# Kernel optimization log

Measured on AMD Instinct MI355X. Metric: run time of the kernel, lower is better.

Reference implementation:

```python
import jax, jax.numpy as jnp
import numpy as np

EMB = 300      # LEN_EMB_VECTOR
FH, FO = 200, 200
GH, GO = 200, 200
HH, HO = 200, 3

def _mlp2(x, w1, b1, w2, b2):
    # relu(Linear) -> relu(Linear), torch Linear: y = x @ W.T + b
    h = jax.nn.relu(x @ w1.T + b1)
    return jax.nn.relu(h @ w2.T + b2)

def setup_inputs() -> dict:
    key = jax.random.key(0)
    ks = jax.random.split(key, 16)
    L1, L2 = 8192, 8192
    def lin(k, out_d, in_d):
        kw, kb = jax.random.split(k)
        s = 1.0 / np.sqrt(in_d)
        w = jax.random.uniform(kw, (out_d, in_d), jnp.float32, -s, s)
        b = jax.random.uniform(kb, (out_d,), jnp.float32, -s, s)
        return w, b
    F_w1, F_b1 = lin(ks[0], FH, EMB)
    F_w2, F_b2 = lin(ks[1], FO, FH)
    G_w1, G_b1 = lin(ks[2], GH, 2 * EMB)
    G_w2, G_b2 = lin(ks[3], GO, GH)
    H_w1, H_b1 = lin(ks[4], HH, 2 * GO)
    H_w2, H_b2 = lin(ks[5], HO, HH)
    sen1 = jax.random.normal(ks[6], (L1, EMB), jnp.float32)
    sen2 = jax.random.normal(ks[7], (L2, EMB), jnp.float32)
    return {"sen1": sen1, "sen2": sen2,
            "F_w1": F_w1, "F_b1": F_b1, "F_w2": F_w2, "F_b2": F_b2,
            "G_w1": G_w1, "G_b1": G_b1, "G_w2": G_w2, "G_b2": G_b2,
            "H_w1": H_w1, "H_b1": H_b1, "H_w2": H_w2, "H_b2": H_b2}

def reference(sen1, sen2, F_w1, F_b1, F_w2, F_b2,
              G_w1, G_b1, G_w2, G_b2, H_w1, H_b1, H_w2, H_b2):
    # F projection of every token in both sentences
    Fa = _mlp2(sen1, F_w1, F_b1, F_w2, F_b2)   # [L1, 200]
    Fb = _mlp2(sen2, F_w1, F_b1, F_w2, F_b2)   # [L2, 200]
    # E matrix of dot products: e_ij = Fa_i . Fb_j
    E = jnp.einsum('id,jd->ij', Fa, Fb)        # [L1, L2]
    # beta_i = softmax over j of E[i, :] applied to sen2
    beta = jax.nn.softmax(E, axis=1) @ sen2    # [L1, EMB]
    # alpha_j = softmax over i of E[:, j] applied to sen1
    alpha = jax.nn.softmax(E, axis=0).T @ sen1 # [L2, EMB]
    # G comparison
    v1 = _mlp2(jnp.concatenate([sen1, beta], axis=-1), G_w1, G_b1, G_w2, G_b2)   # [L1, 200]
    v2 = _mlp2(jnp.concatenate([sen2, alpha], axis=-1), G_w1, G_b1, G_w2, G_b2)  # [L2, 200]
    # aggregate: elementwise sums over tokens, then H classifier with softmax
    hx = jnp.concatenate([v1.sum(axis=0), v2.sum(axis=0)])  # [400]
    logits = jax.nn.relu(hx @ H_w1.T + H_b1) @ H_w2.T + H_b2  # [3]
    return jax.nn.softmax(logits)
```

## Files before the change

kernel.cpp:

```cpp
#include <hip/hip_runtime.h>

typedef __attribute__((ext_vector_type(8))) short short8;
typedef __attribute__((ext_vector_type(4))) float f32x4;

__device__ inline ushort f2bf(float f) {
    union { float f; unsigned u; } v{f};
    unsigned r = v.u + 0x7FFF + ((v.u >> 16) & 1);
    return (ushort)(r >> 16);
}
__device__ inline float bf2f(ushort u) {
    union { unsigned u; float f; } v;
    v.u = ((unsigned)u) << 16;
    return v.f;
}

__device__ inline void gload_lds16(const void* g, void* l) {
    __builtin_amdgcn_global_load_lds(
        (const __attribute__((address_space(1))) unsigned int*)(uintptr_t)g,
        (__attribute__((address_space(3))) unsigned int*)(uintptr_t)l,
        16, 0, 0);
}

__global__ __launch_bounds__(256) void prep_kernel(
    const float* __restrict__ s1, const float* __restrict__ s2,
    const float* __restrict__ W0, const float* __restrict__ b0,
    const float* __restrict__ W1, const float* __restrict__ b1,
    const float* __restrict__ W2, const float* __restrict__ b2,
    const float* __restrict__ W3, const float* __restrict__ b3,
    ushort* __restrict__ Senb, ushort* __restrict__ St1, ushort* __restrict__ St2,
    ushort* __restrict__ Wb0, float* __restrict__ bp0,
    ushort* __restrict__ Wb1, float* __restrict__ bp1,
    ushort* __restrict__ Wb2, float* __restrict__ bp2,
    ushort* __restrict__ Wb3, float* __restrict__ bp3)
{
    const int bid = blockIdx.x;
    if (bid < 896) {
        const int mat = bid / 224, n = bid % 224;
        if (mat == 2) {
            for (int k = threadIdx.x; k < 640; k += 256) {
                float v = 0.f;
                if (n < 200) {
                    if (k < 320) { if (k < 300) v = W2[(size_t)n * 600 + k]; }
                    else { int cc = k - 320; if (cc < 300) v = W2[(size_t)n * 600 + 300 + cc]; }
                }
                Wb2[(size_t)n * 640 + k] = f2bf(v);
            }
            if (threadIdx.x == 0) bp2[n] = (n < 200) ? b2[n] : 0.f;
            return;
        }
        const float* W; const float* b; ushort* Wb; float* bp; int N, K, KP;
        if (mat == 0)      { W = W0; b = b0; Wb = Wb0; bp = bp0; N = 200; K = 300; KP = 320; }
        else if (mat == 1) { W = W1; b = b1; Wb = Wb1; bp = bp1; N = 200; K = 200; KP = 224; }
        else               { W = W3; b = b3; Wb = Wb3; bp = bp3; N = 200; K = 200; KP = 224; }
        for (int k = threadIdx.x; k < KP; k += 256)
            Wb[(size_t)n * KP + k] = (n < N && k < K) ? f2bf(W[(size_t)n * K + k]) : (ushort)0;
        if (threadIdx.x == 0) bp[n] = (n < N) ? b[n] : 0.f;
        return;
    }
    const int sb = bid - 896;
    const int gx = sb & 127;
    const int rest = sb >> 7;
    const int gy = rest % 5, gz = rest / 5;
    const float* X = gz ? s2 : s1;
    ushort* Xt = gz ? St2 : St1;
    ushort* Sb = Senb + (size_t)gz * 8192 * 320;
    __shared__ float t[64][65];
    const int r0 = gx * 64, c0 = gy * 64;
    const int tc = threadIdx.x & 63, tr = threadIdx.x >> 6;
    for (int rr = tr; rr < 64; rr += 4) {
        int c = c0 + tc;
        float v = (c < 300) ? X[(size_t)(r0 + rr) * 300 + c] : 0.f;
        t[rr][tc] = v;
        if (c < 320) Sb[(size_t)(r0 + rr) * 320 + c] = f2bf(v);
    }
    __syncthreads();
    for (int rr = tr; rr < 64; rr += 4) {
        int oc = c0 + rr;
        if (oc < 320)
            Xt[(size_t)oc * 8192 + r0 + tc] = f2bf(t[tc][rr]);
    }
}

__global__ __launch_bounds__(128) void mlp2_kernel(
    const ushort* __restrict__ X,
    const ushort* __restrict__ W1, const float* __restrict__ b1,
    const ushort* __restrict__ W2, const float* __restrict__ b2,
    ushort* __restrict__ Ybf)
{
    const int r0 = blockIdx.x * 16;
    const int tid = threadIdx.x;
    const int wv = tid >> 6;
    const int lane = tid & 63;
    const int lr = lane & 15, lg = lane >> 4;

    __shared__ __align__(16) ushort Y1[16][232];
    __shared__ __align__(16) ushort Pp[16][224];

    f32x4 a1[14];
#pragma unroll
    for (int t = 0; t < 14; ++t) a1[t] = f32x4{0.f, 0.f, 0.f, 0.f};

    const ushort* Xrow = X + (size_t)(r0 + lr) * 320 + lg * 8;
    const ushort* W1r  = W1 + (size_t)lr * 320 + lg * 8;
    const int kb1 = wv * 160;
    for (int k0 = kb1; k0 < kb1 + 160; k0 += 32) {
        short8 a = *(const short8*)(Xrow + k0);
#pragma unroll
        for (int t = 0; t < 14; ++t) {
            short8 bfr = *(const short8*)(W1r + (size_t)t * 16 * 320 + k0);
            a1[t] = __builtin_amdgcn_mfma_f32_16x16x32_bf16(a, bfr, a1[t], 0, 0, 0);
        }
    }
    if (wv == 1) {
#pragma unroll
        for (int t = 0; t < 14; ++t)
#pragma unroll
            for (int rr = 0; rr < 4; ++rr)
                Pp[lg * 4 + rr][t * 16 + lr] = f2bf(a1[t][rr]);
    }
    __syncthreads();
    if (wv == 0) {
#pragma unroll
        for (int t = 0; t < 14; ++t) {
            int col = t * 16 + lr;
            float bv = b1[col];
#pragma unroll
            for (int rr = 0; rr < 4; ++rr) {
                float v = a1[t][rr] + bf2f(Pp[lg * 4 + rr][col]) + bv;
                Y1[lg * 4 + rr][col] = f2bf(fmaxf(v, 0.f));
            }
        }
    }
    __syncthreads();

    f32x4 a2[14];
#pragma unroll
    for (int t = 0; t < 14; ++t) a2[t] = f32x4{0.f, 0.f, 0.f, 0.f};
    const ushort* W2r = W2 + (size_t)lr * 224 + lg * 8;
    const int kb2 = wv * 128, ke2 = wv ? 224 : 128;
    for (int k0 = kb2; k0 < ke2; k0 += 32) {
        short8 a = *(const short8*)&Y1[lr][lg * 8 + k0];
#pragma unroll
        for (int t = 0; t < 14; ++t) {
            short8 bfr = *(const short8*)(W2r + (size_t)t * 16 * 224 + k0);
            a2[t] = __builtin_amdgcn_mfma_f32_16x16x32_bf16(a, bfr, a2[t], 0, 0, 0);
        }
    }
    if (wv == 1) {
#pragma unroll
        for (int t = 0; t < 14; ++t)
#pragma unroll
            for (int rr = 0; rr < 4; ++rr)
                Pp[lg * 4 + rr][t * 16 + lr] = f2bf(a2[t][rr]);
    }
    __syncthreads();
    if (wv == 0) {
#pragma unroll
        for (int t = 0; t < 14; ++t) {
            int col = t * 16 + lr;
            float bv = b2[col];
#pragma unroll
            for (int rr = 0; rr < 4; ++rr) {
                int row = r0 + lg * 4 + rr;
                float v = a2[t][rr] + bf2f(Pp[lg * 4 + rr][col]) + bv;
                Ybf[(size_t)row * 224 + col] = f2bf(fmaxf(v, 0.f));
            }
        }
    }
}

__global__ __launch_bounds__(128) void gmlp2_kernel(
    const ushort* __restrict__ Senb,
    const ushort* __restrict__ Pacc, const float* __restrict__ Dpart,
    const ushort* __restrict__ W1, const float* __restrict__ b1,
    const ushort* __restrict__ W2, const float* __restrict__ b2,
    float* __restrict__ Part)
{
    const int r0 = blockIdx.x * 16;
    const int tid = threadIdx.x;
    const int wv = tid >> 6;
    const int lane = tid & 63;
    const int lr = lane & 15, lg = lane >> 4;
    const int row = r0 + lr;

    __shared__ __align__(16) ushort Y1[16][232];
    __shared__ __align__(16) ushort Pp[16][224];

    f32x4 a1[14];
#pragma unroll
    for (int t = 0; t < 14; ++t) a1[t] = f32x4{0.f, 0.f, 0.f, 0.f};

    const ushort* W1r = W1 + (size_t)lr * 640 + lg * 8;
    if (wv == 0) {
        const ushort* Xrow = Senb + (size_t)row * 320 + lg * 8;
        for (int k0 = 0; k0 < 320; k0 += 32) {
            short8 a = *(const short8*)(Xrow + k0);
#pragma unroll
            for (int t = 0; t < 14; ++t) {
                short8 bfr = *(const short8*)(W1r + (size_t)t * 16 * 640 + k0);
                a1[t] = __builtin_amdgcn_mfma_f32_16x16x32_bf16(a, bfr, a1[t], 0, 0, 0);
            }
        }
    } else {
        const float inv = 1.f / (Dpart[row] + Dpart[16384 + row]);
        const ushort* pa = Pacc + (size_t)row * 320;
        const ushort* pb = pa + (size_t)16384 * 320;
        for (int k0 = 320; k0 < 640; k0 += 32) {
            int kk = k0 - 320 + lg * 8;
            short8 x = *(const short8*)(pa + kk);
            short8 y = *(const short8*)(pb + kk);
            short8 a;
#pragma unroll
            for (int m = 0; m < 8; ++m)
                a[m] = (short)f2bf((bf2f((ushort)x[m]) + bf2f((ushort)y[m])) * inv);
#pragma unroll
            for (int t = 0; t < 14; ++t) {
                short8 bfr = *(const short8*)(W1r + (size_t)t * 16 * 640 + k0);
                a1[t] = __builtin_amdgcn_mfma_f32_16x16x32_bf16(a, bfr, a1[t], 0, 0, 0);
            }
        }
    }
    if (wv == 1) {
#pragma unroll
        for (int t = 0; t < 14; ++t)
#pragma unroll
            for (int rr = 0; rr < 4; ++rr)
                Pp[lg * 4 + rr][t * 16 + lr] = f2bf(a1[t][rr]);
    }
    __syncthreads();
    if (wv == 0) {
#pragma unroll
        for (int t = 0; t < 14; ++t) {
            int col = t * 16 + lr;
            float bv = b1[col];
#pragma unroll
            for (int rr = 0; rr < 4; ++rr) {
                float v = a1[t][rr] + bf2f(Pp[lg * 4 + rr][col]) + bv;
                Y1[lg * 4 + rr][col] = f2bf(fmaxf(v, 0.f));
            }
        }
    }
    __syncthreads();

    f32x4 a2[14];
#pragma unroll
    for (int t = 0; t < 14; ++t) a2[t] = f32x4{0.f, 0.f, 0.f, 0.f};
    const ushort* W2r = W2 + (size_t)lr * 224 + lg * 8;
    const int kb2 = wv * 128, ke2 = wv ? 224 : 128;
    for (int k0 = kb2; k0 < ke2; k0 += 32) {
        short8 a = *(const short8*)&Y1[lr][lg * 8 + k0];
#pragma unroll
        for (int t = 0; t < 14; ++t) {
            short8 bfr = *(const short8*)(W2r + (size_t)t * 16 * 224 + k0);
            a2[t] = __builtin_amdgcn_mfma_f32_16x16x32_bf16(a, bfr, a2[t], 0, 0, 0);
        }
    }
    if (wv == 1) {
#pragma unroll
        for (int t = 0; t < 14; ++t)
#pragma unroll
            for (int rr = 0; rr < 4; ++rr)
                Pp[lg * 4 + rr][t * 16 + lr] = f2bf(a2[t][rr]);
    }
    __syncthreads();
    if (wv == 0) {
#pragma unroll
        for (int t = 0; t < 14; ++t) {
            int col = t * 16 + lr;
            if (col < 200) {
                float bv = b2[col];
                float s = 0.f;
#pragma unroll
                for (int rr = 0; rr < 4; ++rr) {
                    float v = a2[t][rr] + bf2f(Pp[lg * 4 + rr][col]) + bv;
                    s += fmaxf(v, 0.f);
                }
                s += __shfl_xor(s, 16);
                s += __shfl_xor(s, 32);
                if (lg == 0)
                    Part[(size_t)blockIdx.x * 200 + col] = s;
            }
        }
    }
}

__global__ __launch_bounds__(512, 2) void attend_mfma_kernel(
    const ushort* __restrict__ FaFb, const ushort* __restrict__ St1,
    const ushort* __restrict__ St2, ushort* __restrict__ Pacc,
    float* __restrict__ Dpart)
{
    const int b = blockIdx.x;
    const int it  = b & 63;
    const int jh  = (b >> 6) & 1;
    const int dir = b >> 7;
    const ushort* A  = FaFb + (dir ? (size_t)8192 * 224 : 0);
    const ushort* B  = FaFb + (dir ? 0 : (size_t)8192 * 224);
    const ushort* St = dir ? St1 : St2;
    const int ib = it * 128;
    const int jo = jh * 4096;

    const int tid = threadIdx.x;
    const int w = tid >> 6;
    const int wi = w >> 1, wj = w & 1;
    const int dq = w & 3,  ih = w >> 2;
    const int lane = tid & 63;
    const int lr = lane & 15, lg = lane >> 4;

    __shared__ __align__(16) ushort Bl[2][28 * 512];
    __shared__ __align__(16) ushort Sl[2][40 * 512];
    __shared__ __align__(16) ushort Pl[128][76];
    __shared__ float dled[8][32];

    f32x4 acc[4][5];
#pragma unroll
    for (int s = 0; s < 4; ++s)
#pragma unroll
        for (int t = 0; t < 5; ++t) acc[s][t] = f32x4{0.f, 0.f, 0.f, 0.f};
    float dsum[2] = {0.f, 0.f};

    short8 afr[2][7];
#pragma unroll
    for (int si = 0; si < 2; ++si) {
        const ushort* Ar = A + (size_t)(ib + wi * 32 + si * 16 + lr) * 224 + lg * 8;
#pragma unroll
        for (int k = 0; k < 7; ++k) afr[si][k] = *(const short8*)(Ar + k * 32);
    }

    const int nB = (w < 4) ? 4 : 3;
    const int pB = (w < 4) ? (w * 4) : (16 + (w - 4) * 3);
    int boff[4];
#pragma unroll
    for (int q = 0; q < 4; ++q) {
        int p = pB + q;
        boff[q] = ((p / 7) * 16 + lr) * 448 + ((p % 7) * 32 + lg * 8) * 2;
    }
    const char* Bb = (const char*)B + (size_t)jo * 448;

    int soff[5];
#pragma unroll
    for (int q = 0; q < 5; ++q) {
        int p = w * 5 + q;
        int srow = p * 8 + (lane >> 3);
        int sl = (lane & 7) ^ (srow & 7);
        soff[q] = srow * 16384 + sl * 16;
    }
    const char* Sb = (const char*)St + (size_t)jo * 2;

    int prow[5], prow7[5];
#pragma unroll
    for (int t = 0; t < 5; ++t) {
        prow[t] = (dq * 80 + t * 16 + lr) * 128;
        prow7[t] = (dq * 80 + t * 16 + lr) & 7;
    }

#pragma unroll
    for (int q = 0; q < 4; ++q)
        if (q < nB) gload_lds16(Bb + boff[q], &Bl[0][(pB + q) * 512]);
#pragma unroll
    for (int q = 0; q < 5; ++q)
        gload_lds16(Sb + soff[q], &Sl[0][(w * 5 + q) * 512]);
    __syncthreads();

    int buf = 0;
    for (int jb = 0; jb < 4096; jb += 64, buf ^= 1) {
        f32x4 e[2][2];
#pragma unroll
        for (int si = 0; si < 2; ++si)
#pragma unroll
            for (int jt = 0; jt < 2; ++jt) e[si][jt] = f32x4{0.f, 0.f, 0.f, 0.f};
        __builtin_amdgcn_s_setprio(1);
#pragma unroll
        for (int kk = 0; kk < 7; ++kk) {
            short8 b0 = *(const short8*)&Bl[buf][((2 * wj + 0) * 7 + kk) * 512 + lane * 8];
            short8 b1 = *(const short8*)&Bl[buf][((2 * wj + 1) * 7 + kk) * 512 + lane * 8];
            e[0][0] = __builtin_amdgcn_mfma_f32_16x16x32_bf16(b0, afr[0][kk], e[0][0], 0, 0, 0);
            e[1][0] = __builtin_amdgcn_mfma_f32_16x16x32_bf16(b0, afr[1][kk], e[1][0], 0, 0, 0);
            e[0][1] = __builtin_amdgcn_mfma_f32_16x16x32_bf16(b1, afr[0][kk], e[0][1], 0, 0, 0);
            e[1][1] = __builtin_amdgcn_mfma_f32_16x16x32_bf16(b1, afr[1][kk], e[1][1], 0, 0, 0);
        }
        __builtin_amdgcn_s_setprio(0);

#pragma unroll
        for (int si = 0; si < 2; ++si) {
#pragma unroll
            for (int jt = 0; jt < 2; ++jt) {
                float x0 = __expf(e[si][jt][0]);
                float x1 = __expf(e[si][jt][1]);
                float x2 = __expf(e[si][jt][2]);
                float x3 = __expf(e[si][jt][3]);
                dsum[si] += (x0 + x1) + (x2 + x3);
                uint2 pk;
                pk.x = (unsigned)f2bf(x0) | ((unsigned)f2bf(x1) << 16);
                pk.y = (unsigned)f2bf(x2) | ((unsigned)f2bf(x3) << 16);
                *(uint2*)&Pl[wi * 32 + si * 16 + lr][wj * 32 + jt * 16 + lg * 4] = pk;
            }
        }
        __syncthreads();

        if (jb + 64 < 4096) {
            const char* Bn = Bb + (size_t)(jb + 64) * 448;
            const char* Sn = Sb + (size_t)(jb + 64) * 2;
#pragma unroll
            for (int q = 0; q < 4; ++q)
                if (q < nB) gload_lds16(Bn + boff[q], &Bl[buf ^ 1][(pB + q) * 512]);
#pragma unroll
            for (int q = 0; q < 5; ++q)
                gload_lds16(Sn + soff[q], &Sl[buf ^ 1][(w * 5 + q) * 512]);
        }

#pragma unroll
        for (int h = 0; h < 2; ++h) {
            short8 pf[4];
#pragma unroll
            for (int s = 0; s < 4; ++s)
                pf[s] = *(const short8*)&Pl[ih * 64 + s * 16 + lr][h * 32 + lg * 8];
            short8 st[5];
#pragma unroll
            for (int t = 0; t < 5; ++t) {
                int sl = ((h << 2) | lg) ^ prow7[t];
                st[t] = *(const short8*)((const char*)Sl[buf] + prow[t] + (sl << 4));
            }
            __builtin_amdgcn_s_setprio(1);
#pragma unroll
            for (int s = 0; s < 4; ++s)
#pragma unroll
                for (int t = 0; t < 5; ++t)
                    acc[s][t] = __builtin_amdgcn_mfma_f32_16x16x32_bf16(pf[s], st[t], acc[s][t], 0, 0, 0);
            __builtin_amdgcn_s_setprio(0);
        }
        __syncthreads();
    }

#pragma unroll
    for (int si = 0; si < 2; ++si) {
        dsum[si] += __shfl_xor(dsum[si], 16);
        dsum[si] += __shfl_xor(dsum[si], 32);
    }
    if (lg == 0) {
#pragma unroll
        for (int si = 0; si < 2; ++si)
            dled[w][si * 16 + lr] = dsum[si];
    }
    __syncthreads();

    if (tid < 128) {
        int wi2 = tid >> 5, idx = tid & 31;
        Dpart[(size_t)jh * 16384 + dir * 8192 + ib + tid] =
            dled[wi2 * 2][idx] + dled[wi2 * 2 + 1][idx];
    }

    ushort* Pb = Pacc + ((size_t)jh * 16384 + dir * 8192 + ib + ih * 64) * 320;
#pragma unroll
    for (int t = 0; t < 5; ++t) {
        int d = dq * 80 + t * 16 + lr;
#pragma unroll
        for (int s = 0; s < 4; ++s)
#pragma unroll
            for (int r = 0; r < 4; ++r)
                Pb[(size_t)(s * 16 + lg * 4 + r) * 320 + d] = f2bf(acc[s][t][r]);
    }
}

__global__ __launch_bounds__(1024) void tail_kernel(
    const float* __restrict__ Part,
    const float* __restrict__ Hw1, const float* __restrict__ Hb1,
    const float* __restrict__ Hw2, const float* __restrict__ Hb2,
    float* __restrict__ out)
{
    __shared__ float hpart[800];
    __shared__ float hx[400];
    __shared__ float hr[200];
    __shared__ float lgts[3];
    const int tid = threadIdx.x;

    if (tid < 800) {
        int oc = tid >> 1, ph = tid & 1;
        const float* base = Part + ((size_t)((oc < 200 ? 0 : 512) + ph * 256)) * 200 + (oc % 200);
        float s = 0.f;
        for (int q = 0; q < 256; ++q) s += base[(size_t)q * 200];
        hpart[tid] = s;
    }
    __syncthreads();
    if (tid < 400) hx[tid] = hpart[2 * tid] + hpart[2 * tid + 1];
    __syncthreads();

    {
        int r = tid >> 2, p = tid & 3;
        float a = 0.f;
        if (r < 200) {
            for (int kk = 0; kk < 100; ++kk) {
                int k = p + 4 * kk;
                a = fmaf(hx[k], Hw1[r * 400 + k], a);
            }
        }
        a += __shfl_xor(a, 1);
        a += __shfl_xor(a, 2);
        if (p == 0 && r < 200) hr[r] = fmaxf(a + Hb1[r], 0.f);
    }
    __syncthreads();

    if (tid < 192) {
        int o = tid >> 6, ln = tid & 63;
        float a = 0.f;
        for (int k = ln; k < 200; k += 64)
            a = fmaf(hr[k], Hw2[o * 200 + k], a);
#pragma unroll
        for (int m = 1; m < 64; m <<= 1) a += __shfl_xor(a, m);
        if (ln == 0) lgts[o] = a + Hb2[o];
    }
    __syncthreads();
    if (tid == 0) {
        float m = fmaxf(lgts[0], fmaxf(lgts[1], lgts[2]));
        float e0 = __expf(lgts[0] - m);
        float e1 = __expf(lgts[1] - m);
        float e2 = __expf(lgts[2] - m);
        float s = e0 + e1 + e2;
        out[0] = e0 / s;
        out[1] = e1 / s;
        out[2] = e2 / s;
    }
}

extern "C" void kernel_launch(void* const* d_in, const int* in_sizes, int n_in,
                              void* d_out, int out_size, void* d_ws, size_t ws_size,
                              hipStream_t stream)
{
    const float* sen1 = (const float*)d_in[0];
    const float* sen2 = (const float*)d_in[1];
    const float* F_w1 = (const float*)d_in[2];
    const float* F_b1 = (const float*)d_in[3];
    const float* F_w2 = (const float*)d_in[4];
    const float* F_b2 = (const float*)d_in[5];
    const float* G_w1 = (const float*)d_in[6];
    const float* G_b1 = (const float*)d_in[7];
    const float* G_w2 = (const float*)d_in[8];
    const float* G_b2 = (const float*)d_in[9];
    const float* H_w1 = (const float*)d_in[10];
    const float* H_b1 = (const float*)d_in[11];
    const float* H_w2 = (const float*)d_in[12];
    const float* H_b2 = (const float*)d_in[13];
    float* out = (float*)d_out;

    const int L = 8192;
    char* p = (char*)d_ws;
    ushort* St1  = (ushort*)p; p += (size_t)320 * L * 2;
    ushort* St2  = (ushort*)p; p += (size_t)320 * L * 2;
    ushort* Senb = (ushort*)p; p += (size_t)2 * L * 320 * 2;
    ushort* FaFb = (ushort*)p; p += (size_t)2 * L * 224 * 2;
    ushort* WbF1 = (ushort*)p; p += (size_t)224 * 320 * 2;
    ushort* WbF2 = (ushort*)p; p += (size_t)224 * 224 * 2;
    ushort* WbG1 = (ushort*)p; p += (size_t)224 * 640 * 2;
    ushort* WbG2 = (ushort*)p; p += (size_t)224 * 224 * 2;
    float*  bpF1 = (float*)p;  p += 224 * 4;
    float*  bpF2 = (float*)p;  p += 224 * 4;
    float*  bpG1 = (float*)p;  p += 224 * 4;
    float*  bpG2 = (float*)p;  p += 224 * 4;
    ushort* Pacc = (ushort*)p; p += (size_t)2 * 16384 * 320 * 2;
    float*  Dpart= (float*)p;  p += (size_t)2 * 16384 * 4;
    float*  Part = (float*)p;  p += (size_t)1024 * 200 * 4;

    hipLaunchKernelGGL(prep_kernel, dim3(896 + 1280), dim3(256), 0, stream,
                       sen1, sen2,
                       F_w1, F_b1, F_w2, F_b2, G_w1, G_b1, G_w2, G_b2,
                       Senb, St1, St2,
                       WbF1, bpF1, WbF2, bpF2, WbG1, bpG1, WbG2, bpG2);

    hipLaunchKernelGGL(mlp2_kernel, dim3(2 * L / 16), dim3(128), 0, stream,
                       Senb, WbF1, bpF1, WbF2, bpF2, FaFb);

    hipLaunchKernelGGL(attend_mfma_kernel, dim3(256), dim3(512), 0, stream,
                       FaFb, St1, St2, Pacc, Dpart);

    hipLaunchKernelGGL(gmlp2_kernel, dim3(2 * L / 16), dim3(128), 0, stream,
                       Senb, Pacc, Dpart, WbG1, bpG1, WbG2, bpG2, Part);

    hipLaunchKernelGGL(tail_kernel, dim3(1), dim3(1024), 0, stream,
                       Part, H_w1, H_b1, H_w2, H_b2, out);
}
```

Baseline: 280.2 us.

## Split attention key range four ways and use single-wave MLP blocks

The attention kernel now splits the j dimension into four quarters instead of two, doubling the grid to 512 blocks. Partial numerators and denominators are written to four slices and summed in the G MLP. The sentence tile for the PV product is now read straight from global memory into registers instead of being staged through double-buffered LDS, which removes that shared buffer and its async loads. The F and G MLP kernels drop the two-wave K-split and LDS partial-sum exchange in favour of one wave per 16-row block. This trades more partial-buffer traffic and uncoalesced-style register loads for more parallelism and less LDS and synchronisation.

New measurement: 363.9 us. +29.8%, slower.

```diff
diff --git a/kernel.cpp b/kernel.cpp
--- a/kernel.cpp
+++ b/kernel.cpp
@@ -81,20 +81,17 @@
     }
 }
 
-__global__ __launch_bounds__(128) void mlp2_kernel(
+__global__ __launch_bounds__(64) void mlp2_kernel(
     const ushort* __restrict__ X,
     const ushort* __restrict__ W1, const float* __restrict__ b1,
     const ushort* __restrict__ W2, const float* __restrict__ b2,
     ushort* __restrict__ Ybf)
 {
     const int r0 = blockIdx.x * 16;
-    const int tid = threadIdx.x;
-    const int wv = tid >> 6;
-    const int lane = tid & 63;
+    const int lane = threadIdx.x;
     const int lr = lane & 15, lg = lane >> 4;
 
     __shared__ __align__(16) ushort Y1[16][232];
-    __shared__ __align__(16) ushort Pp[16][224];
 
     f32x4 a1[14];
 #pragma unroll
@@ -102,8 +99,7 @@
 
     const ushort* Xrow = X + (size_t)(r0 + lr) * 320 + lg * 8;
     const ushort* W1r  = W1 + (size_t)lr * 320 + lg * 8;
-    const int kb1 = wv * 160;
-    for (int k0 = kb1; k0 < kb1 + 160; k0 += 32) {
+    for (int k0 = 0; k0 < 320; k0 += 32) {
         short8 a = *(const short8*)(Xrow + k0);
 #pragma unroll
         for (int t = 0; t < 14; ++t) {
@@ -111,25 +107,13 @@
             a1[t] = __builtin_amdgcn_mfma_f32_16x16x32_bf16(a, bfr, a1[t], 0, 0, 0);
         }
     }
-    if (wv == 1) {
-#pragma unroll
-        for (int t = 0; t < 14; ++t)
-#pragma unroll
-            for (int rr = 0; rr < 4; ++rr)
-                Pp[lg * 4 + rr][t * 16 + lr] = f2bf(a1[t][rr]);
-    }
-    __syncthreads();
-    if (wv == 0) {
-#pragma unroll
-        for (int t = 0; t < 14; ++t) {
-            int col = t * 16 + lr;
-            float bv = b1[col];
-#pragma unroll
-            for (int rr = 0; rr < 4; ++rr) {
-                float v = a1[t][rr] + bf2f(Pp[lg * 4 + rr][col]) + bv;
-                Y1[lg * 4 + rr][col] = f2bf(fmaxf(v, 0.f));
-            }
-        }
+#pragma unroll
+    for (int t = 0; t < 14; ++t) {
+        int col = t * 16 + lr;
+        float bv = b1[col];
+#pragma unroll
+        for (int rr = 0; rr < 4; ++rr)
+            Y1[lg * 4 + rr][col] = f2bf(fmaxf(a1[t][rr] + bv, 0.f));
     }
     __syncthreads();
 
@@ -137,8 +121,7 @@
 #pragma unroll
     for (int t = 0; t < 14; ++t) a2[t] = f32x4{0.f, 0.f, 0.f, 0.f};
     const ushort* W2r = W2 + (size_t)lr * 224 + lg * 8;
-    const int kb2 = wv * 128, ke2 = wv ? 224 : 128;
-    for (int k0 = kb2; k0 < ke2; k0 += 32) {
+    for (int k0 = 0; k0 < 224; k0 += 32) {
         short8 a = *(const short8*)&Y1[lr][lg * 8 + k0];
 #pragma unroll
         for (int t = 0; t < 14; ++t) {
@@ -146,30 +129,19 @@
             a2[t] = __builtin_amdgcn_mfma_f32_16x16x32_bf16(a, bfr, a2[t], 0, 0, 0);
         }
     }
-    if (wv == 1) {
-#pragma unroll
-        for (int t = 0; t < 14; ++t)
-#pragma unroll
-            for (int rr = 0; rr < 4; ++rr)
-                Pp[lg * 4 + rr][t * 16 + lr] = f2bf(a2[t][rr]);
-    }
-    __syncthreads();
-    if (wv == 0) {
-#pragma unroll
-        for (int t = 0; t < 14; ++t) {
-            int col = t * 16 + lr;
-            float bv = b2[col];
-#pragma unroll
-            for (int rr = 0; rr < 4; ++rr) {
-                int row = r0 + lg * 4 + rr;
-                float v = a2[t][rr] + bf2f(Pp[lg * 4 + rr][col]) + bv;
-                Ybf[(size_t)row * 224 + col] = f2bf(fmaxf(v, 0.f));
-            }
-        }
-    }
-}
-
-__global__ __launch_bounds__(128) void gmlp2_kernel(
+#pragma unroll
+    for (int t = 0; t < 14; ++t) {
+        int col = t * 16 + lr;
+        float bv = b2[col];
+#pragma unroll
+        for (int rr = 0; rr < 4; ++rr) {
+            int row = r0 + lg * 4 + rr;
+            Ybf[(size_t)row * 224 + col] = f2bf(fmaxf(a2[t][rr] + bv, 0.f));
+        }
+    }
+}
+
+__global__ __launch_bounds__(64) void gmlp2_kernel(
     const ushort* __restrict__ Senb,
     const ushort* __restrict__ Pacc, const float* __restrict__ Dpart,
     const ushort* __restrict__ W1, const float* __restrict__ b1,
@@ -177,68 +149,52 @@
     float* __restrict__ Part)
 {
     const int r0 = blockIdx.x * 16;
-    const int tid = threadIdx.x;
-    const int wv = tid >> 6;
-    const int lane = tid & 63;
+    const int lane = threadIdx.x;
     const int lr = lane & 15, lg = lane >> 4;
     const int row = r0 + lr;
 
     __shared__ __align__(16) ushort Y1[16][232];
-    __shared__ __align__(16) ushort Pp[16][224];
+
+    const float inv = 1.f / (Dpart[row] + Dpart[16384 + row] +
+                             Dpart[2 * 16384 + row] + Dpart[3 * 16384 + row]);
+    const ushort* pa = Pacc + (size_t)row * 320;
 
     f32x4 a1[14];
 #pragma unroll
     for (int t = 0; t < 14; ++t) a1[t] = f32x4{0.f, 0.f, 0.f, 0.f};
 
-    const ushort* W1r = W1 + (size_t)lr * 640 + lg * 8;
-    if (wv == 0) {
-        const ushort* Xrow = Senb + (size_t)row * 320 + lg * 8;
-        for (int k0 = 0; k0 < 320; k0 += 32) {
-            short8 a = *(const short8*)(Xrow + k0);
-#pragma unroll
-            for (int t = 0; t < 14; ++t) {
-                short8 bfr = *(const short8*)(W1r + (size_t)t * 16 * 640 + k0);
-                a1[t] = __builtin_amdgcn_mfma_f32_16x16x32_bf16(a, bfr, a1[t], 0, 0, 0);
+    const ushort* Xrow = Senb + (size_t)row * 320 + lg * 8;
+    const ushort* W1r  = W1 + (size_t)lr * 640 + lg * 8;
+    for (int k0 = 0; k0 < 640; k0 += 32) {
+        short8 a;
+        if (k0 < 320) {
+            a = *(const short8*)(Xrow + k0);
+        } else {
+            int kk = k0 - 320 + lg * 8;
+            short8 x0 = *(const short8*)(pa + kk);
+            short8 x1 = *(const short8*)(pa + (size_t)16384 * 320 + kk);
+            short8 x2 = *(const short8*)(pa + (size_t)2 * 16384 * 320 + kk);
+            short8 x3 = *(const short8*)(pa + (size_t)3 * 16384 * 320 + kk);
+#pragma unroll
+            for (int m = 0; m < 8; ++m) {
+                float s = bf2f((ushort)x0[m]) + bf2f((ushort)x1[m]) +
+                          bf2f((ushort)x2[m]) + bf2f((ushort)x3[m]);
+                a[m] = (short)f2bf(s * inv);
             }
         }
-    } else {
-        const float inv = 1.f / (Dpart[row] + Dpart[16384 + row]);
-        const ushort* pa = Pacc + (size_t)row * 320;
-        const ushort* pb = pa + (size_t)16384 * 320;
-        for (int k0 = 320; k0 < 640; k0 += 32) {
-            int kk = k0 - 320 + lg * 8;
-            short8 x = *(const short8*)(pa + kk);
-            short8 y = *(const short8*)(pb + kk);
-            short8 a;
-#pragma unroll
-            for (int m = 0; m < 8; ++m)
-                a[m] = (short)f2bf((bf2f((ushort)x[m]) + bf2f((ushort)y[m])) * inv);
-#pragma unroll
-            for (int t = 0; t < 14; ++t) {
-                short8 bfr = *(const short8*)(W1r + (size_t)t * 16 * 640 + k0);
-                a1[t] = __builtin_amdgcn_mfma_f32_16x16x32_bf16(a, bfr, a1[t], 0, 0, 0);
-            }
-        }
-    }
-    if (wv == 1) {
-#pragma unroll
-        for (int t = 0; t < 14; ++t)
-#pragma unroll
-            for (int rr = 0; rr < 4; ++rr)
-                Pp[lg * 4 + rr][t * 16 + lr] = f2bf(a1[t][rr]);
-    }
-    __syncthreads();
-    if (wv == 0) {
 #pragma unroll
         for (int t = 0; t < 14; ++t) {
-            int col = t * 16 + lr;
-            float bv = b1[col];
-#pragma unroll
-            for (int rr = 0; rr < 4; ++rr) {
-                float v = a1[t][rr] + bf2f(Pp[lg * 4 + rr][col]) + bv;
-                Y1[lg * 4 + rr][col] = f2bf(fmaxf(v, 0.f));
-            }
-        }
+            short8 bfr = *(const short8*)(W1r + (size_t)t * 16 * 640 + k0);
+            a1[t] = __builtin_amdgcn_mfma_f32_16x16x32_bf16(a, bfr, a1[t], 0, 0, 0);
+        }
+    }
+#pragma unroll
+    for (int t = 0; t < 14; ++t) {
+        int col = t * 16 + lr;
+        float bv = b1[col];
+#pragma unroll
+        for (int rr = 0; rr < 4; ++rr)
+            Y1[lg * 4 + rr][col] = f2bf(fmaxf(a1[t][rr] + bv, 0.f));
     }
     __syncthreads();
 
@@ -246,8 +202,7 @@
 #pragma unroll
     for (int t = 0; t < 14; ++t) a2[t] = f32x4{0.f, 0.f, 0.f, 0.f};
     const ushort* W2r = W2 + (size_t)lr * 224 + lg * 8;
-    const int kb2 = wv * 128, ke2 = wv ? 224 : 128;
-    for (int k0 = kb2; k0 < ke2; k0 += 32) {
+    for (int k0 = 0; k0 < 224; k0 += 32) {
         short8 a = *(const short8*)&Y1[lr][lg * 8 + k0];
 #pragma unroll
         for (int t = 0; t < 14; ++t) {
@@ -255,31 +210,19 @@
             a2[t] = __builtin_amdgcn_mfma_f32_16x16x32_bf16(a, bfr, a2[t], 0, 0, 0);
         }
     }
-    if (wv == 1) {
-#pragma unroll
-        for (int t = 0; t < 14; ++t)
+#pragma unroll
+    for (int t = 0; t < 14; ++t) {
+        int col = t * 16 + lr;
+        if (col < 200) {
+            float bv = b2[col];
+            float s = 0.f;
 #pragma unroll
             for (int rr = 0; rr < 4; ++rr)
-                Pp[lg * 4 + rr][t * 16 + lr] = f2bf(a2[t][rr]);
-    }
-    __syncthreads();
-    if (wv == 0) {
-#pragma unroll
-        for (int t = 0; t < 14; ++t) {
-            int col = t * 16 + lr;
-            if (col < 200) {
-                float bv = b2[col];
-                float s = 0.f;
-#pragma unroll
-                for (int rr = 0; rr < 4; ++rr) {
-                    float v = a2[t][rr] + bf2f(Pp[lg * 4 + rr][col]) + bv;
-                    s += fmaxf(v, 0.f);
-                }
-                s += __shfl_xor(s, 16);
-                s += __shfl_xor(s, 32);
-                if (lg == 0)
-                    Part[(size_t)blockIdx.x * 200 + col] = s;
-            }
+                s += fmaxf(a2[t][rr] + bv, 0.f);
+            s += __shfl_xor(s, 16);
+            s += __shfl_xor(s, 32);
+            if (lg == 0)
+                Part[(size_t)blockIdx.x * 200 + col] = s;
         }
     }
 }
@@ -291,13 +234,13 @@
 {
     const int b = blockIdx.x;
     const int it  = b & 63;
-    const int jh  = (b >> 6) & 1;
-    const int dir = b >> 7;
+    const int jq  = (b >> 6) & 3;
+    const int dir = b >> 8;
     const ushort* A  = FaFb + (dir ? (size_t)8192 * 224 : 0);
     const ushort* B  = FaFb + (dir ? 0 : (size_t)8192 * 224);
     const ushort* St = dir ? St1 : St2;
     const int ib = it * 128;
-    const int jo = jh * 4096;
+    const int jo = jq * 2048;
 
     const int tid = threadIdx.x;
     const int w = tid >> 6;
@@ -307,7 +250,6 @@
     const int lr = lane & 15, lg = lane >> 4;
 
     __shared__ __align__(16) ushort Bl[2][28 * 512];
-    __shared__ __align__(16) ushort Sl[2][40 * 512];
     __shared__ __align__(16) ushort Pl[128][76];
     __shared__ float dled[8][32];
 
@@ -336,33 +278,20 @@
     }
     const char* Bb = (const char*)B + (size_t)jo * 448;
 
-    int soff[5];
-#pragma unroll
-    for (int q = 0; q < 5; ++q) {
-        int p = w * 5 + q;
-        int srow = p * 8 + (lane >> 3);
-        int sl = (lane & 7) ^ (srow & 7);
-        soff[q] = srow * 16384 + sl * 16;
-    }
-    const char* Sb = (const char*)St + (size_t)jo * 2;
-
-    int prow[5], prow7[5];
-#pragma unroll
-    for (int t = 0; t < 5; ++t) {
-        prow[t] = (dq * 80 + t * 16 + lr) * 128;
-        prow7[t] = (dq * 80 + t * 16 + lr) & 7;
-    }
+    const ushort* Sbase = St + (size_t)(dq * 80 + lr) * 8192 + jo + lg * 8;
 
 #pragma unroll
     for (int q = 0; q < 4; ++q)
         if (q < nB) gload_lds16(Bb + boff[q], &Bl[0][(pB + q) * 512]);
-#pragma unroll
-    for (int q = 0; q < 5; ++q)
-        gload_lds16(Sb + soff[q], &Sl[0][(w * 5 + q) * 512]);
     __syncthreads();
 
     int buf = 0;
-    for (int jb = 0; jb < 4096; jb += 64, buf ^= 1) {
+    for (int jb = 0; jb < 2048; jb += 64, buf ^= 1) {
+        short8 st0[5];
+#pragma unroll
+        for (int t = 0; t < 5; ++t)
+            st0[t] = *(const short8*)(Sbase + (size_t)t * 16 * 8192 + jb);
+
         f32x4 e[2][2];
 #pragma unroll
         for (int si = 0; si < 2; ++si)
@@ -379,6 +308,11 @@
             e[1][1] = __builtin_amdgcn_mfma_f32_16x16x32_bf16(b1, afr[1][kk], e[1][1], 0, 0, 0);
         }
         __builtin_amdgcn_s_setprio(0);
+
+        short8 st1[5];
+#pragma unroll
+        for (int t = 0; t < 5; ++t)
+            st1[t] = *(const short8*)(Sbase + (size_t)t * 16 * 8192 + jb + 32);
 
 #pragma unroll
         for (int si = 0; si < 2; ++si) {
@@ -397,35 +331,34 @@
         }
         __syncthreads();
 
-        if (jb + 64 < 4096) {
+        if (jb + 64 < 2048) {
             const char* Bn = Bb + (size_t)(jb + 64) * 448;
-            const char* Sn = Sb + (size_t)(jb + 64) * 2;
 #pragma unroll
             for (int q = 0; q < 4; ++q)
                 if (q < nB) gload_lds16(Bn + boff[q], &Bl[buf ^ 1][(pB + q) * 512]);
-#pragma unroll
-            for (int q = 0; q < 5; ++q)
-                gload_lds16(Sn + soff[q], &Sl[buf ^ 1][(w * 5 + q) * 512]);
-        }
-
-#pragma unroll
-        for (int h = 0; h < 2; ++h) {
+        }
+
+        {
             short8 pf[4];
 #pragma unroll
             for (int s = 0; s < 4; ++s)
-                pf[s] = *(const short8*)&Pl[ih * 64 + s * 16 + lr][h * 32 + lg * 8];
-            short8 st[5];
-#pragma unroll
-            for (int t = 0; t < 5; ++t) {
-                int sl = ((h << 2) | lg) ^ prow7[t];
-                st[t] = *(const short8*)((const char*)Sl[buf] + prow[t] + (sl << 4));
-            }
+                pf[s] = *(const short8*)&Pl[ih * 64 + s * 16 + lr][lg * 8];
             __builtin_amdgcn_s_setprio(1);
 #pragma unroll
             for (int s = 0; s < 4; ++s)
 #pragma unroll
                 for (int t = 0; t < 5; ++t)
-                    acc[s][t] = __builtin_amdgcn_mfma_f32_16x16x32_bf16(pf[s], st[t], acc[s][t], 0, 0, 0);
+                    acc[s][t] = __builtin_amdgcn_mfma_f32_16x16x32_bf16(pf[s], st0[t], acc[s][t], 0, 0, 0);
+            __builtin_amdgcn_s_setprio(0);
+#pragma unroll
+            for (int s = 0; s < 4; ++s)
+                pf[s] = *(const short8*)&Pl[ih * 64 + s * 16 + lr][32 + lg * 8];
+            __builtin_amdgcn_s_setprio(1);
+#pragma unroll
+            for (int s = 0; s < 4; ++s)
+#pragma unroll
+                for (int t = 0; t < 5; ++t)
+                    acc[s][t] = __builtin_amdgcn_mfma_f32_16x16x32_bf16(pf[s], st1[t], acc[s][t], 0, 0, 0);
             __builtin_amdgcn_s_setprio(0);
         }
         __syncthreads();
@@ -445,11 +378,11 @@
 
     if (tid < 128) {
         int wi2 = tid >> 5, idx = tid & 31;
-        Dpart[(size_t)jh * 16384 + dir * 8192 + ib + tid] =
+        Dpart[(size_t)jq * 16384 + dir * 8192 + ib + tid] =
             dled[wi2 * 2][idx] + dled[wi2 * 2 + 1][idx];
     }
 
-    ushort* Pb = Pacc + ((size_t)jh * 16384 + dir * 8192 + ib + ih * 64) * 320;
+    ushort* Pb = Pacc + ((size_t)jq * 16384 + dir * 8192 + ib + ih * 64) * 320;
 #pragma unroll
     for (int t = 0; t < 5; ++t) {
         int d = dq * 80 + t * 16 + lr;
@@ -555,8 +488,8 @@
     float*  bpF2 = (float*)p;  p += 224 * 4;
     float*  bpG1 = (float*)p;  p += 224 * 4;
     float*  bpG2 = (float*)p;  p += 224 * 4;
-    ushort* Pacc = (ushort*)p; p += (size_t)2 * 16384 * 320 * 2;
-    float*  Dpart= (float*)p;  p += (size_t)2 * 16384 * 4;
+    ushort* Pacc = (ushort*)p; p += (size_t)4 * 16384 * 320 * 2;
+    float*  Dpart= (float*)p;  p += (size_t)4 * 16384 * 4;
     float*  Part = (float*)p;  p += (size_t)1024 * 200 * 4;
 
     hipLaunchKernelGGL(prep_kernel, dim3(896 + 1280), dim3(256), 0, stream,
@@ -565,13 +498,13 @@
                        Senb, St1, St2,
                        WbF1, bpF1, WbF2, bpF2, WbG1, bpG1, WbG2, bpG2);
 
-    hipLaunchKernelGGL(mlp2_kernel, dim3(2 * L / 16), dim3(128), 0, stream,
+    hipLaunchKernelGGL(mlp2_kernel, dim3(2 * L / 16), dim3(64), 0, stream,
                        Senb, WbF1, bpF1, WbF2, bpF2, FaFb);
 
-    hipLaunchKernelGGL(attend_mfma_kernel, dim3(256), dim3(512), 0, stream,
+    hipLaunchKernelGGL(attend_mfma_kernel, dim3(512), dim3(512), 0, stream,
                        FaFb, St1, St2, Pacc, Dpart);
 
-    hipLaunchKernelGGL(gmlp2_kernel, dim3(2 * L / 16), dim3(128), 0, stream,
+    hipLaunchKernelGGL(gmlp2_kernel, dim3(2 * L / 16), dim3(64), 0, stream,
                        Senb, Pacc, Dpart, WbG1, bpG1, WbG2, bpG2, Part);
 
     hipLaunchKernelGGL(tail_kernel, dim3(1), dim3(1024), 0, stream,
```

## Give each wave its own full-K row tile in the MLP kernels

Applied to the files above, without the earlier changes.

Both the F and G MLP kernels move from a split-K scheme, where two waves shared one 16-row tile and combined partial sums through shared memory with extra barriers and bf16 rounding, to four independent waves per block that each own a 16-row tile across the full K range. This drops the partial-sum exchange, one barrier per layer, and the idle wave during the epilogues, and makes the G kernel's two halves do balanced work. In exchange each wave runs a longer serial K loop and there are a quarter as many blocks. Part is now indexed per tile instead of per block, so the layout the tail kernel reads stays the same.

Result: slower. 287.0 us (+2.4%).

```diff
diff --git a/kernel.cpp b/kernel.cpp
--- a/kernel.cpp
+++ b/kernel.cpp
@@ -81,20 +81,18 @@
     }
 }
 
-__global__ __launch_bounds__(128) void mlp2_kernel(
+__global__ __launch_bounds__(256) void mlp2_kernel(
     const ushort* __restrict__ X,
     const ushort* __restrict__ W1, const float* __restrict__ b1,
     const ushort* __restrict__ W2, const float* __restrict__ b2,
     ushort* __restrict__ Ybf)
 {
-    const int r0 = blockIdx.x * 16;
-    const int tid = threadIdx.x;
-    const int wv = tid >> 6;
-    const int lane = tid & 63;
+    const int wv = threadIdx.x >> 6;
+    const int r0 = (blockIdx.x * 4 + wv) * 16;
+    const int lane = threadIdx.x & 63;
     const int lr = lane & 15, lg = lane >> 4;
 
-    __shared__ __align__(16) ushort Y1[16][232];
-    __shared__ __align__(16) ushort Pp[16][224];
+    __shared__ __align__(16) ushort Y1[4][16][232];
 
     f32x4 a1[14];
 #pragma unroll
@@ -102,8 +100,7 @@
 
     const ushort* Xrow = X + (size_t)(r0 + lr) * 320 + lg * 8;
     const ushort* W1r  = W1 + (size_t)lr * 320 + lg * 8;
-    const int kb1 = wv * 160;
-    for (int k0 = kb1; k0 < kb1 + 160; k0 += 32) {
+    for (int k0 = 0; k0 < 320; k0 += 32) {
         short8 a = *(const short8*)(Xrow + k0);
 #pragma unroll
         for (int t = 0; t < 14; ++t) {
@@ -111,25 +108,13 @@
             a1[t] = __builtin_amdgcn_mfma_f32_16x16x32_bf16(a, bfr, a1[t], 0, 0, 0);
         }
     }
-    if (wv == 1) {
-#pragma unroll
-        for (int t = 0; t < 14; ++t)
-#pragma unroll
-            for (int rr = 0; rr < 4; ++rr)
-                Pp[lg * 4 + rr][t * 16 + lr] = f2bf(a1[t][rr]);
-    }
-    __syncthreads();
-    if (wv == 0) {
-#pragma unroll
-        for (int t = 0; t < 14; ++t) {
-            int col = t * 16 + lr;
-            float bv = b1[col];
-#pragma unroll
-            for (int rr = 0; rr < 4; ++rr) {
-                float v = a1[t][rr] + bf2f(Pp[lg * 4 + rr][col]) + bv;
-                Y1[lg * 4 + rr][col] = f2bf(fmaxf(v, 0.f));
-            }
-        }
+#pragma unroll
+    for (int t = 0; t < 14; ++t) {
+        int col = t * 16 + lr;
+        float bv = b1[col];
+#pragma unroll
+        for (int rr = 0; rr < 4; ++rr)
+            Y1[wv][lg * 4 + rr][col] = f2bf(fmaxf(a1[t][rr] + bv, 0.f));
     }
     __syncthreads();
 
@@ -137,108 +122,77 @@
 #pragma unroll
     for (int t = 0; t < 14; ++t) a2[t] = f32x4{0.f, 0.f, 0.f, 0.f};
     const ushort* W2r = W2 + (size_t)lr * 224 + lg * 8;
-    const int kb2 = wv * 128, ke2 = wv ? 224 : 128;
-    for (int k0 = kb2; k0 < ke2; k0 += 32) {
-        short8 a = *(const short8*)&Y1[lr][lg * 8 + k0];
+    for (int k0 = 0; k0 < 224; k0 += 32) {
+        short8 a = *(const short8*)&Y1[wv][lr][lg * 8 + k0];
 #pragma unroll
         for (int t = 0; t < 14; ++t) {
             short8 bfr = *(const short8*)(W2r + (size_t)t * 16 * 224 + k0);
             a2[t] = __builtin_amdgcn_mfma_f32_16x16x32_bf16(a, bfr, a2[t], 0, 0, 0);
         }
     }
-    if (wv == 1) {
-#pragma unroll
-        for (int t = 0; t < 14; ++t)
-#pragma unroll
-            for (int rr = 0; rr < 4; ++rr)
-                Pp[lg * 4 + rr][t * 16 + lr] = f2bf(a2[t][rr]);
-    }
-    __syncthreads();
-    if (wv == 0) {
-#pragma unroll
-        for (int t = 0; t < 14; ++t) {
-            int col = t * 16 + lr;
-            float bv = b2[col];
-#pragma unroll
-            for (int rr = 0; rr < 4; ++rr) {
-                int row = r0 + lg * 4 + rr;
-                float v = a2[t][rr] + bf2f(Pp[lg * 4 + rr][col]) + bv;
-                Ybf[(size_t)row * 224 + col] = f2bf(fmaxf(v, 0.f));
-            }
-        }
-    }
-}
-
-__global__ __launch_bounds__(128) void gmlp2_kernel(
+#pragma unroll
+    for (int t = 0; t < 14; ++t) {
+        int col = t * 16 + lr;
+        float bv = b2[col];
+#pragma unroll
+        for (int rr = 0; rr < 4; ++rr) {
+            int row = r0 + lg * 4 + rr;
+            Ybf[(size_t)row * 224 + col] = f2bf(fmaxf(a2[t][rr] + bv, 0.f));
+        }
+    }
+}
+
+__global__ __launch_bounds__(256) void gmlp2_kernel(
     const ushort* __restrict__ Senb,
     const ushort* __restrict__ Pacc, const float* __restrict__ Dpart,
     const ushort* __restrict__ W1, const float* __restrict__ b1,
     const ushort* __restrict__ W2, const float* __restrict__ b2,
     float* __restrict__ Part)
 {
-    const int r0 = blockIdx.x * 16;
-    const int tid = threadIdx.x;
-    const int wv = tid >> 6;
-    const int lane = tid & 63;
+    const int wv = threadIdx.x >> 6;
+    const int tile = blockIdx.x * 4 + wv;
+    const int r0 = tile * 16;
+    const int lane = threadIdx.x & 63;
     const int lr = lane & 15, lg = lane >> 4;
     const int row = r0 + lr;
 
-    __shared__ __align__(16) ushort Y1[16][232];
-    __shared__ __align__(16) ushort Pp[16][224];
+    __shared__ __align__(16) ushort Y1[4][16][232];
+
+    const float inv = 1.f / (Dpart[row] + Dpart[16384 + row]);
+    const ushort* pa = Pacc + (size_t)row * 320;
+    const ushort* pb = pa + (size_t)16384 * 320;
 
     f32x4 a1[14];
 #pragma unroll
     for (int t = 0; t < 14; ++t) a1[t] = f32x4{0.f, 0.f, 0.f, 0.f};
 
-    const ushort* W1r = W1 + (size_t)lr * 640 + lg * 8;
-    if (wv == 0) {
-        const ushort* Xrow = Senb + (size_t)row * 320 + lg * 8;
-        for (int k0 = 0; k0 < 320; k0 += 32) {
-            short8 a = *(const short8*)(Xrow + k0);
-#pragma unroll
-            for (int t = 0; t < 14; ++t) {
-                short8 bfr = *(const short8*)(W1r + (size_t)t * 16 * 640 + k0);
-                a1[t] = __builtin_amdgcn_mfma_f32_16x16x32_bf16(a, bfr, a1[t], 0, 0, 0);
-            }
-        }
-    } else {
-        const float inv = 1.f / (Dpart[row] + Dpart[16384 + row]);
-        const ushort* pa = Pacc + (size_t)row * 320;
-        const ushort* pb = pa + (size_t)16384 * 320;
-        for (int k0 = 320; k0 < 640; k0 += 32) {
+    const ushort* Xrow = Senb + (size_t)row * 320 + lg * 8;
+    const ushort* W1r  = W1 + (size_t)lr * 640 + lg * 8;
+    for (int k0 = 0; k0 < 640; k0 += 32) {
+        short8 a;
+        if (k0 < 320) {
+            a = *(const short8*)(Xrow + k0);
+        } else {
             int kk = k0 - 320 + lg * 8;
             short8 x = *(const short8*)(pa + kk);
             short8 y = *(const short8*)(pb + kk);
-            short8 a;
 #pragma unroll
             for (int m = 0; m < 8; ++m)
                 a[m] = (short)f2bf((bf2f((ushort)x[m]) + bf2f((ushort)y[m])) * inv);
-#pragma unroll
-            for (int t = 0; t < 14; ++t) {
-                short8 bfr = *(const short8*)(W1r + (size_t)t * 16 * 640 + k0);
-                a1[t] = __builtin_amdgcn_mfma_f32_16x16x32_bf16(a, bfr, a1[t], 0, 0, 0);
-            }
-        }
-    }
-    if (wv == 1) {
-#pragma unroll
-        for (int t = 0; t < 14; ++t)
-#pragma unroll
-            for (int rr = 0; rr < 4; ++rr)
-                Pp[lg * 4 + rr][t * 16 + lr] = f2bf(a1[t][rr]);
-    }
-    __syncthreads();
-    if (wv == 0) {
+        }
 #pragma unroll
         for (int t = 0; t < 14; ++t) {
-            int col = t * 16 + lr;
-            float bv = b1[col];
-#pragma unroll
-            for (int rr = 0; rr < 4; ++rr) {
-                float v = a1[t][rr] + bf2f(Pp[lg * 4 + rr][col]) + bv;
-                Y1[lg * 4 + rr][col] = f2bf(fmaxf(v, 0.f));
-            }
-        }
+            short8 bfr = *(const short8*)(W1r + (size_t)t * 16 * 640 + k0);
+            a1[t] = __builtin_amdgcn_mfma_f32_16x16x32_bf16(a, bfr, a1[t], 0, 0, 0);
+        }
+    }
+#pragma unroll
+    for (int t = 0; t < 14; ++t) {
+        int col = t * 16 + lr;
+        float bv = b1[col];
+#pragma unroll
+        for (int rr = 0; rr < 4; ++rr)
+            Y1[wv][lg * 4 + rr][col] = f2bf(fmaxf(a1[t][rr] + bv, 0.f));
     }
     __syncthreads();
 
@@ -246,40 +200,27 @@
 #pragma unroll
     for (int t = 0; t < 14; ++t) a2[t] = f32x4{0.f, 0.f, 0.f, 0.f};
     const ushort* W2r = W2 + (size_t)lr * 224 + lg * 8;
-    const int kb2 = wv * 128, ke2 = wv ? 224 : 128;
-    for (int k0 = kb2; k0 < ke2; k0 += 32) {
-        short8 a = *(const short8*)&Y1[lr][lg * 8 + k0];
+    for (int k0 = 0; k0 < 224; k0 += 32) {
+        short8 a = *(const short8*)&Y1[wv][lr][lg * 8 + k0];
 #pragma unroll
         for (int t = 0; t < 14; ++t) {
             short8 bfr = *(const short8*)(W2r + (size_t)t * 16 * 224 + k0);
             a2[t] = __builtin_amdgcn_mfma_f32_16x16x32_bf16(a, bfr, a2[t], 0, 0, 0);
         }
     }
-    if (wv == 1) {
-#pragma unroll
-        for (int t = 0; t < 14; ++t)
+#pragma unroll
+    for (int t = 0; t < 14; ++t) {
+        int col = t * 16 + lr;
+        if (col < 200) {
+            float bv = b2[col];
+            float s = 0.f;
 #pragma unroll
             for (int rr = 0; rr < 4; ++rr)
-                Pp[lg * 4 + rr][t * 16 + lr] = f2bf(a2[t][rr]);
-    }
-    __syncthreads();
-    if (wv == 0) {
-#pragma unroll
-        for (int t = 0; t < 14; ++t) {
-            int col = t * 16 + lr;
-            if (col < 200) {
-                float bv = b2[col];
-                float s = 0.f;
-#pragma unroll
-                for (int rr = 0; rr < 4; ++rr) {
-                    float v = a2[t][rr] + bf2f(Pp[lg * 4 + rr][col]) + bv;
-                    s += fmaxf(v, 0.f);
-                }
-                s += __shfl_xor(s, 16);
-                s += __shfl_xor(s, 32);
-                if (lg == 0)
-                    Part[(size_t)blockIdx.x * 200 + col] = s;
-            }
+                s += fmaxf(a2[t][rr] + bv, 0.f);
+            s += __shfl_xor(s, 16);
+            s += __shfl_xor(s, 32);
+            if (lg == 0)
+                Part[(size_t)tile * 200 + col] = s;
         }
     }
 }
@@ -565,13 +506,13 @@
                        Senb, St1, St2,
                        WbF1, bpF1, WbF2, bpF2, WbG1, bpG1, WbG2, bpG2);
 
-    hipLaunchKernelGGL(mlp2_kernel, dim3(2 * L / 16), dim3(128), 0, stream,
+    hipLaunchKernelGGL(mlp2_kernel, dim3(2 * L / 64), dim3(256), 0, stream,
                        Senb, WbF1, bpF1, WbF2, bpF2, FaFb);
 
     hipLaunchKernelGGL(attend_mfma_kernel, dim3(256), dim3(512), 0, stream,
                        FaFb, St1, St2, Pacc, Dpart);
 
-    hipLaunchKernelGGL(gmlp2_kernel, dim3(2 * L / 16), dim3(128), 0, stream,
+    hipLaunchKernelGGL(gmlp2_kernel, dim3(2 * L / 64), dim3(256), 0, stream,
                        Senb, Pacc, Dpart, WbG1, bpG1, WbG2, bpG2, Part);
 
     hipLaunchKernelGGL(tail_kernel, dim3(1), dim3(1024), 0, stream,
```
